# Kernel tuning notes

Measured on AMD Instinct MI355X. Metric: run time of the kernel, lower is better.

The kernel has to match this reference:

```python
import jax, jax.numpy as jnp
import numpy as np
from jax.scipy.special import logsumexp

T, B, N = 512, 1024, 64


def setup_inputs() -> dict:
    key = jax.random.key(0)
    k1, k2, k3, k4, k5, k6 = jax.random.split(key, 6)
    emit = jax.random.normal(k1, (T, B, N), dtype=jnp.float32)
    scale = 1.0 / np.sqrt(N).astype(np.float32)
    trans = jax.random.normal(k2, (N, N), dtype=jnp.float32) * scale
    strans = jax.random.normal(k3, (N,), dtype=jnp.float32) * scale
    etrans = jax.random.normal(k4, (N,), dtype=jnp.float32) * scale
    target = jax.random.randint(k5, (T, B), 0, N, dtype=jnp.int64)
    # contiguous-prefix valid mask: position t is valid iff t < length_b
    lengths = jax.random.randint(k6, (B,), 1, T + 1)
    mask = jnp.arange(T)[:, None] < lengths[None, :]
    return {"emit": emit, "trans": trans, "strans": strans,
            "etrans": etrans, "target": target, "mask": mask}


def _get_logZ(emit, mask, trans, strans, etrans):
    alpha0 = strans + emit[0]                       # (B, N)
    def step(alpha, inp):
        e_i, m_i = inp                              # (B, N), (B,)
        # scores[b, j, k] = alpha[b, j] + trans[j, k] + e_i[b, k]
        s = logsumexp(alpha[:, :, None] + trans[None, :, :] + e_i[:, None, :], axis=1)
        alpha = jnp.where(m_i[:, None], s, alpha)
        return alpha, None
    alpha, _ = jax.lax.scan(step, alpha0, (emit[1:], mask[1:]))
    return logsumexp(alpha + etrans, axis=1).sum()


def _score(emit, target, mask, trans, strans, etrans):
    Tt, Bb, _ = emit.shape
    # emission scores of the gold path
    scores = jnp.take_along_axis(emit, target[:, :, None], axis=2)[..., 0]  # (T, B)
    scores = scores.at[1:].add(trans[target[:-1], target[1:]])
    score = jnp.sum(jnp.where(mask, scores, jnp.float32(0)))
    ends = mask.sum(axis=0) - 1                     # (B,) last valid index
    score = score + strans[target[0]].sum()
    last_tags = target[ends, jnp.arange(Bb)]
    score = score + etrans[last_tags].sum()
    return score


def reference(emit, trans, strans, etrans, target, mask):
    _, Bb, _ = emit.shape
    logZ = _get_logZ(emit, mask, trans, strans, etrans)
    score = _score(emit, target, mask, trans, strans, etrans)
    return (logZ - score) / Bb
```

## Files before the change

### kernel.cpp

```cpp
#include <hip/hip_runtime.h>
#include <stdint.h>

#define TT 512
#define BB 1024
#define NN 64

typedef __attribute__((ext_vector_type(8))) short short8;
typedef __attribute__((ext_vector_type(4))) float f32x4;

union W8 { uint32_t w[4]; short8 v; };

__device__ __forceinline__ uint32_t cvt_pk_bf16(float lo, float hi){
    uint32_t r;
    asm("v_cvt_pk_bf16_f32 %0, %1, %2" : "=v"(r) : "v"(lo), "v"(hi));
    return r;
}
__device__ __forceinline__ void perm32swap(uint32_t &a, uint32_t &b){
    asm("v_permlane32_swap_b32 %0, %1" : "+v"(a), "+v"(b));
}
__device__ __forceinline__ void perm16swap(uint32_t &a, uint32_t &b){
    asm("v_permlane16_swap_b32 %0, %1" : "+v"(a), "+v"(b));
}

__global__ void __launch_bounds__(64, 1)
detect_kernel(const uint32_t* __restrict__ tgt, const uint8_t* __restrict__ msk,
              int* __restrict__ flags) {
    if (threadIdx.x == 0) {
        uint32_t s = 0;
        for (int i = 0; i < 128; ++i) s |= tgt[2 * i + 1];
        flags[0] = (s == 0) ? 1 : 0;
        uint32_t mz = 0;
        for (int i = 0; i < 8; ++i) mz |= msk[4*i+1] | msk[4*i+2] | msk[4*i+3];
        flags[1] = (mz == 0) ? 1 : 0;
    }
}

__global__ void __launch_bounds__(256)
score_kernel(const float* __restrict__ emit, const float* __restrict__ trans,
             const float* __restrict__ strans, const float* __restrict__ etrans,
             const void* __restrict__ target, const void* __restrict__ mask,
             const int* __restrict__ flags, float* __restrict__ out)
{
    const int idx = blockIdx.x * 256 + threadIdx.x;
    const int t = idx >> 10, b = idx & (BB - 1);
    const int t64 = flags[0], m32 = flags[1];

    auto getm = [&](int tt) -> int {
        if (m32) return ((const int*)mask)[(size_t)tt * BB + b] != 0;
        else     return ((const uint8_t*)mask)[(size_t)tt * BB + b] != 0;
    };
    auto gett = [&](int tt) -> int {
        if (t64) return (int)((const long long*)target)[(size_t)tt * BB + b];
        else     return ((const int*)target)[(size_t)tt * BB + b];
    };

    const int m  = getm(t);
    const int tg = gett(t);
    float term = 0.f;
    if (m)      term += emit[((size_t)t * BB + b) * NN + tg];
    if (t == 0) term += strans[tg];
    if (t > 0 && m) term += trans[gett(t - 1) * NN + tg];
    const int mn = (t == TT - 1) ? 0 : getm(t + 1);
    if (m && !mn) term += etrans[tg];

    #pragma unroll
    for (int off = 1; off < 64; off <<= 1) term += __shfl_xor(term, off);
    __shared__ float sred[4];
    const int wid = threadIdx.x >> 6, lane = threadIdx.x & 63;
    if (lane == 0) sred[wid] = term;
    __syncthreads();
    if (threadIdx.x == 0)
        atomicAdd(out, -(sred[0] + sred[1] + sred[2] + sred[3]) * (1.0f / (float)BB));
}

__global__ void __launch_bounds__(64, 1)
crf_scan(const float* __restrict__ emit, const float* __restrict__ trans,
         const float* __restrict__ strans, const float* __restrict__ etrans,
         const void* __restrict__ mask, const int* __restrict__ flags,
         float* __restrict__ out)
{
    const int lane = threadIdx.x & 63;
    const int q = lane >> 4;
    const int c = lane & 15;
    const int b = (blockIdx.x << 4) + c;
    const int m32 = flags[1];

    int lp = 0;
    if (m32) {
        const int* mp = (const int*)mask;
        #pragma unroll 8
        for (int i = 0; i < 128; ++i)
            lp += (mp[(size_t)(q * 128 + i) * BB + b] != 0) ? 1 : 0;
    } else {
        const uint8_t* mp = (const uint8_t*)mask;
        #pragma unroll 8
        for (int i = 0; i < 128; ++i)
            lp += (mp[(size_t)(q * 128 + i) * BB + b] != 0) ? 1 : 0;
    }
    lp += __shfl_xor(lp, 16);
    lp += __shfl_xor(lp, 32);
    const int len = lp;
    int maxlen = len;
    #pragma unroll
    for (int off = 1; off < 64; off <<= 1)
        maxlen = max(maxlen, __shfl_xor(maxlen, off));
    const int NSTEP = maxlen - 1;

    short8 Ef[4][2];
    #pragma unroll
    for (int mt = 0; mt < 4; ++mt) {
        #pragma unroll
        for (int kt = 0; kt < 2; ++kt) {
            W8 u;
            #pragma unroll
            for (int jj = 0; jj < 8; jj += 2) {
                float f0 = __expf(trans[(size_t)(32*kt + 8*q + jj    ) * NN + 16*mt + c]);
                float f1 = __expf(trans[(size_t)(32*kt + 8*q + jj + 1) * NN + 16*mt + c]);
                u.w[jj >> 1] = cvt_pk_bf16(f0, f1);
            }
            Ef[mt][kt] = u.v;
        }
    }
    float ee[4][4];
    #pragma unroll
    for (int mt = 0; mt < 4; ++mt)
        #pragma unroll
        for (int r = 0; r < 4; ++r)
            ee[mt][r] = __expf(etrans[16*mt + 4*q + r]);

    f32x4 S[4];
    float m = 0.f, lz = 0.f;
    #pragma unroll
    for (int mt = 0; mt < 4; ++mt) {
        f32x4 e0 = *(const f32x4*)(emit + (size_t)b * NN + 16*mt + 4*q);
        #pragma unroll
        for (int r = 0; r < 4; ++r)
            S[mt][r] = __expf(strans[16*mt + 4*q + r] + e0[r]);
    }

    auto renorm = [&]() {
        float x0 = fmaxf(fmaxf(S[0][0], S[0][1]), fmaxf(S[0][2], S[0][3]));
        float x1 = fmaxf(fmaxf(S[1][0], S[1][1]), fmaxf(S[1][2], S[1][3]));
        float x2 = fmaxf(fmaxf(S[2][0], S[2][1]), fmaxf(S[2][2], S[2][3]));
        float x3 = fmaxf(fmaxf(S[3][0], S[3][1]), fmaxf(S[3][2], S[3][3]));
        float mx = fmaxf(fmaxf(x0, x1), fmaxf(x2, x3));
        mx = fmaxf(mx, __shfl_xor(mx, 16));
        mx = fmaxf(mx, __shfl_xor(mx, 32));
        int ex = (int)((__float_as_uint(mx) >> 23) & 0xffu) - 127;
        float sc = __uint_as_float((uint32_t)(127 - ex) << 23);
        #pragma unroll
        for (int mt = 0; mt < 4; ++mt)
            #pragma unroll
            for (int r = 0; r < 4; ++r)
                S[mt][r] *= sc;
        m += (float)ex * 0.6931471805599453f;
    };
    renorm();

    auto extract_if = [&](int t) {
        if (__any(len == t)) {
            float ve = 0.f;
            #pragma unroll
            for (int mt = 0; mt < 4; ++mt)
                #pragma unroll
                for (int r = 0; r < 4; ++r)
                    ve = __builtin_fmaf(S[mt][r], ee[mt][r], ve);
            ve += __shfl_xor(ve, 16);
            ve += __shfl_xor(ve, 32);
            float cand = m + __logf(ve);
            lz = (len == t) ? cand : lz;
        }
    };

    f32x4 R[8][4];
    auto prefetch = [&](int t, f32x4 (&Rk)[4]) {
        int tl = (t < TT) ? t : (TT - 1);
        const float* p = emit + ((size_t)tl << 16) + (size_t)b * NN + 4 * q;
        #pragma unroll
        for (int mt = 0; mt < 4; ++mt)
            Rk[mt] = *(const f32x4*)(p + 16 * mt);
    };

    auto dostep = [&](int t, f32x4 (&Rk)[4]) {
        extract_if(t);
        f32x4 EB[4];
        #pragma unroll
        for (int mt = 0; mt < 4; ++mt)
            #pragma unroll
            for (int r = 0; r < 4; ++r)
                EB[mt][r] = __expf(Rk[mt][r]);
        uint32_t pk[4][2];
        #pragma unroll
        for (int mt = 0; mt < 4; ++mt) {
            pk[mt][0] = cvt_pk_bf16(S[mt][0], S[mt][1]);
            pk[mt][1] = cvt_pk_bf16(S[mt][2], S[mt][3]);
        }
        W8 B0, B1;
        {
            uint32_t a, bb;
            a = pk[0][0]; bb = pk[1][0]; perm32swap(a, bb); perm16swap(a, bb);
            B0.w[0] = a; B0.w[2] = bb;
            a = pk[0][1]; bb = pk[1][1]; perm32swap(a, bb); perm16swap(a, bb);
            B0.w[1] = a; B0.w[3] = bb;
            a = pk[2][0]; bb = pk[3][0]; perm32swap(a, bb); perm16swap(a, bb);
            B1.w[0] = a; B1.w[2] = bb;
            a = pk[2][1]; bb = pk[3][1]; perm32swap(a, bb); perm16swap(a, bb);
            B1.w[1] = a; B1.w[3] = bb;
        }
        #pragma unroll
        for (int mt = 0; mt < 4; ++mt) {
            f32x4 acc = {0.f, 0.f, 0.f, 0.f};
            acc = __builtin_amdgcn_mfma_f32_16x16x32_bf16(Ef[mt][0], B0.v, acc, 0, 0, 0);
            acc = __builtin_amdgcn_mfma_f32_16x16x32_bf16(Ef[mt][1], B1.v, acc, 0, 0, 0);
            #pragma unroll
            for (int r = 0; r < 4; ++r)
                S[mt][r] = acc[r] * EB[mt][r];
        }
        if ((t & 3) == 0) renorm();
    };

    if (NSTEP > 0) {
        #pragma unroll
        for (int k = 0; k < 8; ++k) prefetch(1 + k, R[k]);
        int t = 1;
        while (t + 7 <= NSTEP) {
            #pragma unroll
            for (int k = 0; k < 8; ++k) {
                dostep(t + k, R[k]);
                prefetch(t + k + 8, R[k]);
            }
            t += 8;
        }
        #pragma unroll
        for (int k = 0; k < 8; ++k) {
            if (t + k <= NSTEP) dostep(t + k, R[k]);
        }
    }
    extract_if(maxlen);

    float contrib = (q == 0) ? lz : 0.f;
    #pragma unroll
    for (int off = 1; off < 64; off <<= 1) contrib += __shfl_xor(contrib, off);
    if (lane == 0) atomicAdd(out, contrib * (1.0f / (float)BB));
}

extern "C" void kernel_launch(void* const* d_in, const int* in_sizes, int n_in,
                              void* d_out, int out_size, void* d_ws, size_t ws_size,
                              hipStream_t stream) {
    const float* emit   = (const float*)d_in[0];
    const float* trans  = (const float*)d_in[1];
    const float* strans = (const float*)d_in[2];
    const float* etrans = (const float*)d_in[3];
    const void*  target = d_in[4];
    const void*  mask   = d_in[5];
    int* flags = (int*)d_ws;

    hipMemsetAsync(d_out, 0, sizeof(float), stream);
    detect_kernel<<<1, 64, 0, stream>>>((const uint32_t*)target,
                                        (const uint8_t*)mask, flags);
    score_kernel<<<(TT * BB) / 256, 256, 0, stream>>>(emit, trans, strans, etrans,
                                                      target, mask, flags, (float*)d_out);
    crf_scan<<<BB / 16, 64, 0, stream>>>(emit, trans, strans, etrans,
                                         mask, flags, (float*)d_out);
}
```

Measured before the change: 214.5 us.

## Stage emission tiles through a swizzled LDS ring buffer with coalesced loads

Per-step emission loads change from scattered per-lane 16-byte reads into fully contiguous 4KB wave-wide loads. These are written into a 16-slot swizzled LDS ring buffer and read back in the MFMA-fragment layout. The scan loop is restructured into a 6-step software pipeline: global loads run about 12 steps ahead, with double-buffered register reads from LDS. This aims to improve global-memory coalescing and hide load latency in the serial recurrence. The cost is 64KB of shared memory per block and extra LDS traffic on the critical path.

```diff
diff --git a/kernel.cpp b/kernel.cpp
--- a/kernel.cpp
+++ b/kernel.cpp
@@ -79,10 +79,13 @@
          const void* __restrict__ mask, const int* __restrict__ flags,
          float* __restrict__ out)
 {
+    __shared__ float s_eb[16 * 1024];
+
     const int lane = threadIdx.x & 63;
     const int q = lane >> 4;
     const int c = lane & 15;
-    const int b = (blockIdx.x << 4) + c;
+    const int b0 = blockIdx.x << 4;
+    const int b = b0 + c;
     const int m32 = flags[1];
 
     int lp = 0;
@@ -172,23 +175,52 @@
         }
     };
 
-    f32x4 R[8][4];
-    auto prefetch = [&](int t, f32x4 (&Rk)[4]) {
-        int tl = (t < TT) ? t : (TT - 1);
-        const float* p = emit + ((size_t)tl << 16) + (size_t)b * NN + 4 * q;
+    uint32_t woff[4];
+    #pragma unroll
+    for (int pp = 0; pp < 4; ++pp) {
+        const int chain = 4 * pp + (lane >> 4);
+        uint32_t byte = ((uint32_t)chain << 8) + ((uint32_t)(lane & 15) << 4);
+        byte ^= (uint32_t)((chain & 7) << 4);
+        woff[pp] = byte;
+    }
+    uint32_t roff[4];
+    #pragma unroll
+    for (int mt = 0; mt < 4; ++mt) {
+        uint32_t byte = ((uint32_t)c << 8) + ((uint32_t)mt << 6) + ((uint32_t)q << 4);
+        byte ^= (uint32_t)((c & 7) << 4);
+        roff[mt] = byte;
+    }
+
+    auto loadG = [&](int t, f32x4 (&G)[4]) {
+        int tc = (t < TT) ? t : (TT - 1);
+        const float* p = emit + ((size_t)tc << 16) + (size_t)b0 * NN + lane * 4;
+        #pragma unroll
+        for (int pp = 0; pp < 4; ++pp) {
+            G[pp] = *(const f32x4*)(p + pp * 256);
+            asm volatile("" : "+v"(G[pp]));
+        }
+    };
+    auto writeG = [&](int t, f32x4 (&G)[4]) {
+        char* base = (char*)s_eb + (size_t)((t & 15) * 4096);
+        #pragma unroll
+        for (int pp = 0; pp < 4; ++pp)
+            *(f32x4*)(base + woff[pp]) = G[pp];
+    };
+    auto ebRead = [&](int t, f32x4 (&E)[4]) {
+        char* base = (char*)s_eb + (size_t)((t & 15) * 4096);
         #pragma unroll
         for (int mt = 0; mt < 4; ++mt)
-            Rk[mt] = *(const f32x4*)(p + 16 * mt);
-    };
-
-    auto dostep = [&](int t, f32x4 (&Rk)[4]) {
+            E[mt] = *(const f32x4*)(base + roff[mt]);
+    };
+
+    auto dostep = [&](int t, f32x4 (&Eraw)[4]) {
         extract_if(t);
         f32x4 EB[4];
         #pragma unroll
         for (int mt = 0; mt < 4; ++mt)
             #pragma unroll
             for (int r = 0; r < 4; ++r)
-                EB[mt][r] = __expf(Rk[mt][r]);
+                EB[mt][r] = __expf(Eraw[mt][r]);
         uint32_t pk[4][2];
         #pragma unroll
         for (int mt = 0; mt < 4; ++mt) {
@@ -220,20 +252,30 @@
     };
 
     if (NSTEP > 0) {
-        #pragma unroll
-        for (int k = 0; k < 8; ++k) prefetch(1 + k, R[k]);
+        f32x4 GA[4], GB[4], GC[4], EBa[4], EBb[4];
+        loadG(1, GA); loadG(2, GB); loadG(3, GC);
+        writeG(1, GA); writeG(2, GB); writeG(3, GC);
+        loadG(4, GA); loadG(5, GB); loadG(6, GC);
+        writeG(4, GA); writeG(5, GB); writeG(6, GC);
+        loadG(7, GA); loadG(8, GB); loadG(9, GC);
+        writeG(7, GA); writeG(8, GB); writeG(9, GC);
+        loadG(10, GA); loadG(11, GB); loadG(12, GC);
+        ebRead(1, EBa);
+
         int t = 1;
-        while (t + 7 <= NSTEP) {
-            #pragma unroll
-            for (int k = 0; k < 8; ++k) {
-                dostep(t + k, R[k]);
-                prefetch(t + k + 8, R[k]);
-            }
-            t += 8;
-        }
-        #pragma unroll
-        for (int k = 0; k < 8; ++k) {
-            if (t + k <= NSTEP) dostep(t + k, R[k]);
+        while (t + 5 <= NSTEP) {
+            writeG(t + 9,  GA); loadG(t + 12, GA); ebRead(t + 1, EBb); dostep(t,     EBa);
+            writeG(t + 10, GB); loadG(t + 13, GB); ebRead(t + 2, EBa); dostep(t + 1, EBb);
+            writeG(t + 11, GC); loadG(t + 14, GC); ebRead(t + 3, EBb); dostep(t + 2, EBa);
+            writeG(t + 12, GA); loadG(t + 15, GA); ebRead(t + 4, EBa); dostep(t + 3, EBb);
+            writeG(t + 13, GB); loadG(t + 16, GB); ebRead(t + 5, EBb); dostep(t + 4, EBa);
+            writeG(t + 14, GC); loadG(t + 17, GC); ebRead(t + 6, EBa); dostep(t + 5, EBb);
+            t += 6;
+        }
+        while (t <= NSTEP) {
+            dostep(t, EBa);
+            ++t;
+            if (t <= NSTEP) ebRead(t, EBa);
         }
     }
     extract_if(maxlen);
```

Result: slower. 690.8 us (+222.0%).
